# Optimization experiments

Hardware: AMD Instinct MI355X
Metric: run time of the kernel (lower is better)

## Reference

```python
import jax, jax.numpy as jnp
import numpy as np

N_NODES = 100000
D_FEAT = 128
N_EDGES = 600000


def setup_inputs() -> dict:
    key = jax.random.key(0)
    k_h, k_s, k_d = jax.random.split(key, 3)
    h = jax.random.normal(k_h, (N_NODES, D_FEAT), dtype=jnp.float32)
    src = jax.random.randint(k_s, (N_EDGES,), 0, N_NODES, dtype=jnp.int64)
    dst = jax.random.randint(k_d, (N_EDGES,), 0, N_NODES, dtype=jnp.int64)
    return {"h": h, "src": src, "dst": dst}


def reference(h, src, dst):
    # u_dot_v: per-edge dot product of gathered node features -> [E, 1]
    score = jnp.sum(h[src] * h[dst], axis=-1, keepdims=True)
    # min/max computed on detached scores in the original (numpy detach)
    mn = jax.lax.stop_gradient(jnp.min(score))
    mx = jax.lax.stop_gradient(jnp.max(score))
    norm = (score - mn) / (mx - mn)
    # python loop in original: 0 stays 0, anything else -> 1 (binary threshold)
    out = jnp.where(norm == 0, jnp.zeros_like(norm), jnp.ones_like(norm))
    return out
```

## Files before the change

### kernel.cpp

```cpp
#include <hip/hip_runtime.h>
#include <hip/hip_fp16.h>
#include <float.h>


#define MARGIN 12.0f

__device__ __forceinline__ unsigned enc_key(float f) {
    unsigned u = __float_as_uint(f);
    return (u & 0x80000000u) ? ~u : (u | 0x80000000u);
}
__device__ __forceinline__ float dec_key(unsigned k) {
    unsigned u = (k & 0x80000000u) ? (k ^ 0x80000000u) : ~k;
    return __uint_as_float(u);
}
__device__ __forceinline__ unsigned f2e5m2(float f) {
    unsigned short hb = __builtin_bit_cast(unsigned short, __float2half(f));
    unsigned r = 0x7Fu + ((hb >> 8) & 1u);
    return (((unsigned)hb + r) >> 8) & 0xFFu;
}
__device__ __forceinline__ __half2 h2lo(unsigned u) {
    return __builtin_bit_cast(__half2, __builtin_amdgcn_perm(u, 0u, 0x050C040Cu));
}
__device__ __forceinline__ __half2 h2hi(unsigned u) {
    return __builtin_bit_cast(__half2, __builtin_amdgcn_perm(u, 0u, 0x070C060Cu));
}
__device__ __forceinline__ float dot16(uint4 A, uint4 B) {
    __half2 acc = __builtin_bit_cast(__half2, 0u);
    acc = __hfma2(h2lo(A.x), h2lo(B.x), acc);
    acc = __hfma2(h2hi(A.x), h2hi(B.x), acc);
    acc = __hfma2(h2lo(A.y), h2lo(B.y), acc);
    acc = __hfma2(h2hi(A.y), h2hi(B.y), acc);
    acc = __hfma2(h2lo(A.z), h2lo(B.z), acc);
    acc = __hfma2(h2hi(A.z), h2hi(B.z), acc);
    acc = __hfma2(h2lo(A.w), h2lo(B.w), acc);
    acc = __hfma2(h2hi(A.w), h2hi(B.w), acc);
    return __low2float(acc) + __high2float(acc);
}

__global__ void __launch_bounds__(256) convert_kernel(
    const float4* __restrict__ in, unsigned* __restrict__ outb, int n4) {
    const int stride = gridDim.x * blockDim.x;
    for (int i = blockIdx.x * blockDim.x + threadIdx.x; i < n4; i += stride) {
        float4 f = in[i];
        outb[i] = f2e5m2(f.x) | (f2e5m2(f.y) << 8) |
                  (f2e5m2(f.z) << 16) | (f2e5m2(f.w) << 24);
    }
}

__global__ void __launch_bounds__(256) edge_dot_fp8_kernel(
    const uint4* __restrict__ hb4,
    const int* __restrict__ src,
    const int* __restrict__ dst,
    float* __restrict__ score,
    unsigned int* __restrict__ keys,
    int nEdges) {
    const int tid  = threadIdx.x;
    const int lane = tid & 63;
    const int oct  = lane >> 3;
    const int l8   = lane & 7;
    const int wid  = blockIdx.x * (blockDim.x >> 6) + (tid >> 6);
    const int nW   = gridDim.x * (blockDim.x >> 6);

    float localMin = FLT_MAX;
    const int nG = nEdges >> 4;
    for (int g = wid; g < nG; g += nW) {
        const int e = g << 4;
        const int sA0 = src[e + oct];
        const int sA1 = src[e + 8 + oct];
        const int sB0 = dst[e + oct];
        const int sB1 = dst[e + 8 + oct];
        const uint4 A0 = hb4[(size_t)sA0 * 8 + l8];
        const uint4 A1 = hb4[(size_t)sA1 * 8 + l8];
        const uint4 B0 = hb4[(size_t)sB0 * 8 + l8];
        const uint4 B1 = hb4[(size_t)sB1 * 8 + l8];

        float v0 = dot16(A0, B0);
        float v1 = dot16(A1, B1);
        #pragma unroll
        for (int off = 1; off < 8; off <<= 1) {
            v0 += __shfl_xor(v0, off, 64);
            v1 += __shfl_xor(v1, off, 64);
        }
        if (l8 == 0) {
            score[e + oct]     = v0;
            score[e + 8 + oct] = v1;
        }
        localMin = fminf(localMin, fminf(v0, v1));
    }

    for (int e = (nG << 4) + wid; e < nEdges; e += nW) {
        const uint4 a = hb4[(size_t)src[e] * 8 + l8];
        const uint4 b = hb4[(size_t)dst[e] * 8 + l8];
        float v = dot16(a, b);
        #pragma unroll
        for (int off = 1; off < 8; off <<= 1) v += __shfl_xor(v, off, 64);
        if (lane == 0) score[e] = v;
        localMin = fminf(localMin, v);
    }

    #pragma unroll
    for (int off = 32; off > 0; off >>= 1)
        localMin = fminf(localMin, __shfl_xor(localMin, off, 64));
    __shared__ float red[4];
    if (lane == 0) red[tid >> 6] = localMin;
    __syncthreads();
    if (tid == 0) {
        float m = fminf(fminf(red[0], red[1]), fminf(red[2], red[3]));
        atomicMin(keys, enc_key(m));
    }
}

__global__ void __launch_bounds__(256) refine_kernel(
    const float* __restrict__ h,
    const int* __restrict__ src,
    const int* __restrict__ dst,
    float* __restrict__ score,
    unsigned int* __restrict__ keys,
    int nEdges) {
    const float thresh = dec_key(keys[0]) + MARGIN;
    const int stride = gridDim.x * blockDim.x;
    for (int e = blockIdx.x * blockDim.x + threadIdx.x; e < nEdges; e += stride) {
        float s = score[e];
        if (s <= thresh) {
            const float* ra = h + (size_t)src[e] * 128;
            const float* rb = h + (size_t)dst[e] * 128;
            float acc = 0.0f;
            #pragma unroll 4
            for (int i = 0; i < 128; ++i) acc = fmaf(ra[i], rb[i], acc);
            score[e] = acc;
            atomicMin(keys + 1, enc_key(acc));
        }
    }
}

__global__ void __launch_bounds__(256) threshold_kernel(
    float4* __restrict__ out,
    const unsigned int* __restrict__ keys,
    int n4) {
    const float emin = dec_key(keys[1]);
    const int stride = gridDim.x * blockDim.x;
    for (int i = blockIdx.x * blockDim.x + threadIdx.x; i < n4; i += stride) {
        float4 v = out[i];
        v.x = (v.x == emin) ? 0.0f : 1.0f;
        v.y = (v.y == emin) ? 0.0f : 1.0f;
        v.z = (v.z == emin) ? 0.0f : 1.0f;
        v.w = (v.w == emin) ? 0.0f : 1.0f;
        out[i] = v;
    }
}

__global__ void __launch_bounds__(256) edge_dot_f32_kernel(
    const float* __restrict__ h,
    const int* __restrict__ src,
    const int* __restrict__ dst,
    float* __restrict__ score,
    unsigned int* __restrict__ keys,
    int nEdges) {
    const int lane = threadIdx.x & 63;
    const int wid  = blockIdx.x * (blockDim.x >> 6) + (threadIdx.x >> 6);
    const int nW   = gridDim.x * (blockDim.x >> 6);
    float localMin = FLT_MAX;
    const int nG = nEdges >> 3;
    for (int g = wid; g < nG; g += nW) {
        const int e = g << 3;
        const int4 s0 = *reinterpret_cast<const int4*>(src + e);
        const int4 s1 = *reinterpret_cast<const int4*>(src + e + 4);
        const int4 d0 = *reinterpret_cast<const int4*>(dst + e);
        const int4 d1 = *reinterpret_cast<const int4*>(dst + e + 4);
        const int si[8] = {s0.x,s0.y,s0.z,s0.w,s1.x,s1.y,s1.z,s1.w};
        const int di[8] = {d0.x,d0.y,d0.z,d0.w,d1.x,d1.y,d1.z,d1.w};
        float2 a[8], b[8];
        #pragma unroll
        for (int k = 0; k < 8; ++k) {
            a[k] = *reinterpret_cast<const float2*>(h + (size_t)si[k] * 128 + lane * 2);
            b[k] = *reinterpret_cast<const float2*>(h + (size_t)di[k] * 128 + lane * 2);
        }
        #pragma unroll
        for (int k = 0; k < 8; ++k) {
            float v = fmaf(a[k].y, b[k].y, a[k].x * b[k].x);
            #pragma unroll
            for (int off = 32; off > 0; off >>= 1) v += __shfl_xor(v, off, 64);
            if (lane == 0) score[e + k] = v;
            localMin = fminf(localMin, v);
        }
    }
    for (int e = (nG << 3) + wid; e < nEdges; e += nW) {
        const float2 a = *reinterpret_cast<const float2*>(h + (size_t)src[e] * 128 + lane * 2);
        const float2 b = *reinterpret_cast<const float2*>(h + (size_t)dst[e] * 128 + lane * 2);
        float v = fmaf(a.y, b.y, a.x * b.x);
        #pragma unroll
        for (int off = 32; off > 0; off >>= 1) v += __shfl_xor(v, off, 64);
        if (lane == 0) score[e] = v;
        localMin = fminf(localMin, v);
    }
    if (lane == 0) atomicMin(keys + 1, enc_key(localMin));
}

extern "C" void kernel_launch(void* const* d_in, const int* in_sizes, int n_in,
                              void* d_out, int out_size, void* d_ws, size_t ws_size,
                              hipStream_t stream) {
    const float* h  = (const float*)d_in[0];
    const int* src  = (const int*)d_in[1];
    const int* dst  = (const int*)d_in[2];
    float* out      = (float*)d_out;
    unsigned* keys  = (unsigned*)d_ws;
    const int nH     = in_sizes[0];
    const int nEdges = in_sizes[1];
    const int n4     = nEdges >> 2;

    hipMemsetAsync(d_ws, 0xFF, 8, stream);

    const size_t need = 256 + (size_t)nH;
    if (ws_size >= need && (nEdges & 3) == 0 && (nH & 3) == 0) {
        unsigned* hb = (unsigned*)((char*)d_ws + 256);
        convert_kernel<<<2048, 256, 0, stream>>>(
            (const float4*)h, hb, nH >> 2);
        edge_dot_fp8_kernel<<<2048, 256, 0, stream>>>(
            (const uint4*)hb, src, dst, out, keys, nEdges);
        refine_kernel<<<1024, 256, 0, stream>>>(h, src, dst, out, keys, nEdges);
    } else {
        edge_dot_f32_kernel<<<2048, 256, 0, stream>>>(h, src, dst, out, keys, nEdges);
    }

    int blocks = (n4 + 255) / 256;
    if (blocks > 2048) blocks = 2048;
    threshold_kernel<<<blocks, 256, 0, stream>>>(
        reinterpret_cast<float4*>(out), keys, n4);
}
```

Measured before the change: 136.3 us.

## Replace full threshold pass with candidate list and single-block finalize

The approximate kernel now writes 1.0 to every output directly and keeps approximate scores in a workspace buffer. Refine appends exact candidate values to a compacted list via an atomic counter, and a one-block finalize zeroes only the minimal entries. This removes the full-array threshold read/write pass. It also widens the refine margin, which may add refine work and contention on the atomic counter.

```diff
diff --git a/kernel.cpp b/kernel.cpp
--- a/kernel.cpp
+++ b/kernel.cpp
@@ -3,7 +3,7 @@
 #include <float.h>
 
 
-#define MARGIN 12.0f
+#define MARGIN 20.0f
 
 __device__ __forceinline__ unsigned enc_key(float f) {
     unsigned u = __float_as_uint(f);
@@ -37,6 +37,8 @@
     return __low2float(acc) + __high2float(acc);
 }
 
+struct Cand { unsigned idx; float val; };
+
 __global__ void __launch_bounds__(256) convert_kernel(
     const float4* __restrict__ in, unsigned* __restrict__ outb, int n4) {
     const int stride = gridDim.x * blockDim.x;
@@ -51,7 +53,8 @@
     const uint4* __restrict__ hb4,
     const int* __restrict__ src,
     const int* __restrict__ dst,
-    float* __restrict__ score,
+    float* __restrict__ out1,
+    float* __restrict__ scoreA,
     unsigned int* __restrict__ keys,
     int nEdges) {
     const int tid  = threadIdx.x;
@@ -82,8 +85,10 @@
             v1 += __shfl_xor(v1, off, 64);
         }
         if (l8 == 0) {
-            score[e + oct]     = v0;
-            score[e + 8 + oct] = v1;
+            scoreA[e + oct]     = v0;
+            scoreA[e + 8 + oct] = v1;
+            out1[e + oct]       = 1.0f;
+            out1[e + 8 + oct]   = 1.0f;
         }
         localMin = fminf(localMin, fminf(v0, v1));
     }
@@ -94,7 +99,7 @@
         float v = dot16(a, b);
         #pragma unroll
         for (int off = 1; off < 8; off <<= 1) v += __shfl_xor(v, off, 64);
-        if (lane == 0) score[e] = v;
+        if (lane == 0) { scoreA[e] = v; out1[e] = 1.0f; }
         localMin = fminf(localMin, v);
     }
 
@@ -114,38 +119,41 @@
     const float* __restrict__ h,
     const int* __restrict__ src,
     const int* __restrict__ dst,
-    float* __restrict__ score,
+    const float* __restrict__ scoreA,
     unsigned int* __restrict__ keys,
+    Cand* __restrict__ cand,
     int nEdges) {
     const float thresh = dec_key(keys[0]) + MARGIN;
     const int stride = gridDim.x * blockDim.x;
     for (int e = blockIdx.x * blockDim.x + threadIdx.x; e < nEdges; e += stride) {
-        float s = score[e];
-        if (s <= thresh) {
-            const float* ra = h + (size_t)src[e] * 128;
-            const float* rb = h + (size_t)dst[e] * 128;
+        if (scoreA[e] <= thresh) {
+            const float4* ra = reinterpret_cast<const float4*>(h + (size_t)src[e] * 128);
+            const float4* rb = reinterpret_cast<const float4*>(h + (size_t)dst[e] * 128);
             float acc = 0.0f;
-            #pragma unroll 4
-            for (int i = 0; i < 128; ++i) acc = fmaf(ra[i], rb[i], acc);
-            score[e] = acc;
+            #pragma unroll 8
+            for (int i = 0; i < 32; ++i) {
+                float4 a = ra[i], b = rb[i];
+                acc = fmaf(a.x, b.x, acc);
+                acc = fmaf(a.y, b.y, acc);
+                acc = fmaf(a.z, b.z, acc);
+                acc = fmaf(a.w, b.w, acc);
+            }
+            unsigned slot = atomicAdd(keys + 2, 1u);
+            cand[slot].idx = (unsigned)e;
+            cand[slot].val = acc;
             atomicMin(keys + 1, enc_key(acc));
         }
     }
 }
 
-__global__ void __launch_bounds__(256) threshold_kernel(
-    float4* __restrict__ out,
+__global__ void __launch_bounds__(256) finalize_kernel(
+    float* __restrict__ out,
     const unsigned int* __restrict__ keys,
-    int n4) {
-    const float emin = dec_key(keys[1]);
-    const int stride = gridDim.x * blockDim.x;
-    for (int i = blockIdx.x * blockDim.x + threadIdx.x; i < n4; i += stride) {
-        float4 v = out[i];
-        v.x = (v.x == emin) ? 0.0f : 1.0f;
-        v.y = (v.y == emin) ? 0.0f : 1.0f;
-        v.z = (v.z == emin) ? 0.0f : 1.0f;
-        v.w = (v.w == emin) ? 0.0f : 1.0f;
-        out[i] = v;
+    const Cand* __restrict__ cand) {
+    const unsigned n  = keys[2];
+    const unsigned mk = keys[1];
+    for (unsigned i = threadIdx.x; i < n; i += blockDim.x) {
+        if (enc_key(cand[i].val) == mk) out[cand[i].idx] = 0.0f;
     }
 }
 
@@ -196,6 +204,22 @@
     if (lane == 0) atomicMin(keys + 1, enc_key(localMin));
 }
 
+__global__ void __launch_bounds__(256) threshold_kernel(
+    float4* __restrict__ out,
+    const unsigned int* __restrict__ keys,
+    int n4) {
+    const float emin = dec_key(keys[1]);
+    const int stride = gridDim.x * blockDim.x;
+    for (int i = blockIdx.x * blockDim.x + threadIdx.x; i < n4; i += stride) {
+        float4 v = out[i];
+        v.x = (v.x == emin) ? 0.0f : 1.0f;
+        v.y = (v.y == emin) ? 0.0f : 1.0f;
+        v.z = (v.z == emin) ? 0.0f : 1.0f;
+        v.w = (v.w == emin) ? 0.0f : 1.0f;
+        out[i] = v;
+    }
+}
+
 extern "C" void kernel_launch(void* const* d_in, const int* in_sizes, int n_in,
                               void* d_out, int out_size, void* d_ws, size_t ws_size,
                               hipStream_t stream) {
@@ -206,24 +230,31 @@
     unsigned* keys  = (unsigned*)d_ws;
     const int nH     = in_sizes[0];
     const int nEdges = in_sizes[1];
-    const int n4     = nEdges >> 2;
+
+    const size_t hbOff    = 256;
+    const size_t scoreOff = (hbOff + (size_t)nH + 255) & ~(size_t)255;
+    const size_t candOff  = (scoreOff + (size_t)nEdges * 4 + 255) & ~(size_t)255;
+    const size_t need     = candOff + (size_t)nEdges * 8;
 
     hipMemsetAsync(d_ws, 0xFF, 8, stream);
-
-    const size_t need = 256 + (size_t)nH;
+    hipMemsetAsync((char*)d_ws + 8, 0, 4, stream);
+
     if (ws_size >= need && (nEdges & 3) == 0 && (nH & 3) == 0) {
-        unsigned* hb = (unsigned*)((char*)d_ws + 256);
-        convert_kernel<<<2048, 256, 0, stream>>>(
-            (const float4*)h, hb, nH >> 2);
+        unsigned* hb   = (unsigned*)((char*)d_ws + hbOff);
+        float* scoreA  = (float*)((char*)d_ws + scoreOff);
+        Cand* cand     = (Cand*)((char*)d_ws + candOff);
+        convert_kernel<<<2048, 256, 0, stream>>>((const float4*)h, hb, nH >> 2);
         edge_dot_fp8_kernel<<<2048, 256, 0, stream>>>(
-            (const uint4*)hb, src, dst, out, keys, nEdges);
-        refine_kernel<<<1024, 256, 0, stream>>>(h, src, dst, out, keys, nEdges);
+            (const uint4*)hb, src, dst, out, scoreA, keys, nEdges);
+        refine_kernel<<<1024, 256, 0, stream>>>(
+            h, src, dst, scoreA, keys, cand, nEdges);
+        finalize_kernel<<<1, 256, 0, stream>>>(out, keys, cand);
     } else {
         edge_dot_f32_kernel<<<2048, 256, 0, stream>>>(h, src, dst, out, keys, nEdges);
-    }
-
-    int blocks = (n4 + 255) / 256;
-    if (blocks > 2048) blocks = 2048;
-    threshold_kernel<<<blocks, 256, 0, stream>>>(
-        reinterpret_cast<float4*>(out), keys, n4);
-}
+        const int n4 = nEdges >> 2;
+        int blocks = (n4 + 255) / 256;
+        if (blocks > 2048) blocks = 2048;
+        threshold_kernel<<<blocks, 256, 0, stream>>>(
+            reinterpret_cast<float4*>(out), keys, n4);
+    }
+}
```

Result: slower. 144.9 us (+6.3%).
